# Optimization experiments

Measured on AMD Instinct MI355X. Metric: run time of the kernel, lower is better.

## Reference

```python
import jax, jax.numpy as jnp
import numpy as np

N_NODES = 100_000
N_EDGES = 1_200_000
C = 64            # channel_count
NF = 3            # node features
EF = 2            # edge features
ITERS = 5         # message passing iterations
VAR_EPS = 1e-5


def _mlp(x, W1, b1, W2, b2):
    # NeuralNetwork(in, out, hidden_count=1, hidden_size): in->hidden, relu, hidden->out
    return jax.nn.relu(x @ W1 + b1) @ W2 + b2


def setup_inputs() -> dict:
    key = jax.random.key(0)
    ks = jax.random.split(key, 20)

    def glorot(k, shape):
        fan_in = shape[0]
        return jax.random.normal(k, shape, dtype=jnp.float32) / jnp.sqrt(jnp.float32(fan_in))

    msg_in = EF + 2 * C           # 130
    upd_in = 4 * C + C            # 320 (4 aggregators + node embedding)
    ro_in = 2 * C + EF            # 130

    return {
        "node_features": jax.random.normal(ks[0], (N_NODES, NF), dtype=jnp.float32),
        "edge_features": jax.random.normal(ks[1], (N_EDGES, EF), dtype=jnp.float32),
        "init_W": glorot(ks[2], (NF, C)),
        "init_b": jnp.zeros((C,), jnp.float32),
        "msg_W1": glorot(ks[3], (msg_in, C)),
        "msg_b1": jnp.zeros((C,), jnp.float32),
        "msg_W2": glorot(ks[4], (C, C)),
        "msg_b2": jnp.zeros((C,), jnp.float32),
        "upd_W1": glorot(ks[5], (upd_in, C)),
        "upd_b1": jnp.zeros((C,), jnp.float32),
        "upd_W2": glorot(ks[6], (C, C)),
        "upd_b2": jnp.zeros((C,), jnp.float32),
        "ro_W1": glorot(ks[7], (ro_in, C)),
        "ro_b1": jnp.zeros((C,), jnp.float32),
        "ro_W2": glorot(ks[8], (C, 1)),
        "ro_b2": jnp.zeros((1,), jnp.float32),
        "edge_index": jax.random.randint(ks[9], (2, N_EDGES), 0, N_NODES, dtype=jnp.int32),
    }


def reference(node_features, edge_features, init_W, init_b,
              msg_W1, msg_b1, msg_W2, msg_b2,
              upd_W1, upd_b1, upd_W2, upd_b2,
              ro_W1, ro_b1, ro_W2, ro_b2, edge_index):
    src = edge_index[0]  # j: sender
    dst = edge_index[1]  # i: receiver (PyG source_to_target flow)

    ones = jnp.ones((src.shape[0], 1), jnp.float32)
    cnt = jax.ops.segment_sum(ones, dst, num_segments=N_NODES)      # [N,1]
    cnt_c = jnp.maximum(cnt, 1.0)
    has_edge = cnt > 0

    emb = node_features @ init_W + init_b  # [N,C]
    for _ in range(ITERS):
        h = jax.nn.relu(emb)
        # message: cat(x_i, x_j, edge_features) -> MLP
        m = _mlp(jnp.concatenate([h[dst], h[src], edge_features], axis=1),
                 msg_W1, msg_b1, msg_W2, msg_b2)                    # [E,C]
        s = jax.ops.segment_sum(m, dst, num_segments=N_NODES)
        mean = s / cnt_c
        mean2 = jax.ops.segment_sum(m * m, dst, num_segments=N_NODES) / cnt_c
        std = jnp.sqrt(jax.nn.relu(mean2 - mean * mean) + VAR_EPS)
        mn = jnp.where(has_edge, jax.ops.segment_min(m, dst, num_segments=N_NODES), 0.0)
        mx = jnp.where(has_edge, jax.ops.segment_max(m, dst, num_segments=N_NODES), 0.0)
        agg = jnp.concatenate([std, mn, mx, mean], axis=1)           # [N,4C]
        # update: cat(aggregated, node_embeddings) -> MLP
        emb = _mlp(jnp.concatenate([agg, h], axis=1),
                   upd_W1, upd_b1, upd_W2, upd_b2)

    # readout per edge: cat(emb[attacker], emb[attacked], edge_features)
    ro_in = jnp.concatenate([emb[src], emb[dst], edge_features], axis=1)
    return _mlp(ro_in, ro_W1, ro_b1, ro_W2, ro_b2)                   # [E,1]
```

## Files before the change

### kernel.cpp

```cpp
#include <hip/hip_runtime.h>

#define NN 100000
#define NE 1200000
#define ITERS 5
#define NTILES (NE/16)
#define TPW 16
#define NWAVES ((NTILES+TPW-1)/TPW)
#define NBLK_E ((NWAVES+3)/4)
#define NBLK_U ((NN+63)/64)

typedef __attribute__((ext_vector_type(8))) short short8;
typedef __attribute__((ext_vector_type(4))) short short4_t;
typedef __attribute__((ext_vector_type(4))) float floatx4;
typedef unsigned short ushort_t;

__device__ inline ushort_t f2bf(float f){
  unsigned u = __float_as_uint(f);
  unsigned r = (u + 0x7fffu + ((u>>16)&1u)) >> 16;
  return (ushort_t)r;
}
__device__ inline float bf2f(ushort_t u){ return __uint_as_float(((unsigned)u)<<16); }
__device__ inline float bf2f_lo(unsigned u){ return __uint_as_float(u<<16); }
__device__ inline float bf2f_hi(unsigned u){ return __uint_as_float(u & 0xffff0000u); }

__device__ inline int xcd_swz(int orig, int nwg){
  int q = nwg >> 3, r = nwg & 7;
  int x = orig & 7, i = orig >> 3;
  return (x < r ? x*(q+1) : r*(q+1) + (x-r)*q) + i;
}

__global__ void k_count(const int* __restrict__ dst, int* __restrict__ cnt){
  int base = (blockIdx.x*256 + threadIdx.x)*4;
  if (base >= NE) return;
  int4 d4 = *reinterpret_cast<const int4*>(dst + base);
  atomicAdd(&cnt[d4.x],1); atomicAdd(&cnt[d4.y],1);
  atomicAdd(&cnt[d4.z],1); atomicAdd(&cnt[d4.w],1);
}

__global__ void k_scan1(const int* __restrict__ cnt, int* __restrict__ bsum){
  __shared__ int s[256];
  int t = threadIdx.x; int i = blockIdx.x*256 + t;
  s[t] = (i < NN) ? cnt[i] : 0; __syncthreads();
  for (int off=128; off>0; off>>=1){ if (t<off) s[t]+=s[t+off]; __syncthreads(); }
  if (t==0) bsum[blockIdx.x] = s[0];
}

__global__ void k_scan2(int* bsum, int nb){
  __shared__ int s[512];
  int t = threadIdx.x;
  int v = (t<nb)? bsum[t] : 0;
  s[t]=v; __syncthreads();
  for (int off=1; off<512; off<<=1){
    int x = (t>=off)? s[t-off] : 0; __syncthreads();
    s[t]+=x; __syncthreads();
  }
  if (t<nb) bsum[t] = s[t]-v;
}

__global__ void k_scan3(const int* __restrict__ cnt, const int* __restrict__ bsum, int* __restrict__ rowptr){
  __shared__ int s[256];
  int t=threadIdx.x; int i = blockIdx.x*256+t;
  int v = (i<NN)? cnt[i]:0;
  s[t]=v; __syncthreads();
  for (int off=1; off<256; off<<=1){
    int x = (t>=off)? s[t-off] : 0; __syncthreads();
    s[t] += x; __syncthreads();
  }
  if (i<NN) rowptr[i] = bsum[blockIdx.x] + s[t] - v;
  if (i==0) rowptr[NN] = NE;
}

__global__ void k_filldst(const int* __restrict__ rowptr, int* __restrict__ dsts){
  int n = blockIdx.x*256 + threadIdx.x;
  if (n >= NN) return;
  int a = rowptr[n], b = rowptr[n+1];
  for (int p = a; p < b; ++p) dsts[p] = n;
}

__global__ void k_scatter(const int* __restrict__ src, const int* __restrict__ dst,
                          const float* __restrict__ ef,
                          int* __restrict__ fill,
                          int2* __restrict__ edges){
  int e = blockIdx.x*256+threadIdx.x;
  if (e>=NE) return;
  int d = dst[e];
  float2 f = reinterpret_cast<const float2*>(ef)[e];
  int sv = src[e];
  int pos = atomicAdd(&fill[d],1);
  edges[pos] = make_int2(sv, (int)((unsigned)f2bf(f.x)|((unsigned)f2bf(f.y)<<16)));
}

__global__ void k_wprep(const float* __restrict__ W, ushort_t* __restrict__ frag, int Ksrc, int total){
  int t = blockIdx.x*256+threadIdx.x;
  if (t>=total) return;
  int j = t&7, l=(t>>3)&63, ct=(t>>9)&3, ks=t>>11;
  int k = ks*32 + ((l>>4)<<3) + j;
  int col = ct*16 + (l&15);
  float v = (k<Ksrc)? W[k*64+col] : 0.f;
  frag[t] = f2bf(v);
}

__global__ void k_init(const float* __restrict__ nf, const float* __restrict__ W, const float* __restrict__ b,
                       ushort_t* __restrict__ hA, ushort_t* __restrict__ emb){
  int t = blockIdx.x*256+threadIdx.x;
  if (t >= NN*64) return;
  int n=t>>6, c=t&63;
  float a = b[c];
  a += nf[n*3+0]*W[0*64+c];
  a += nf[n*3+1]*W[1*64+c];
  a += nf[n*3+2]*W[2*64+c];
  emb[t] = f2bf(a);
  hA[t] = f2bf(fmaxf(a,0.f));
}

__launch_bounds__(256)
__global__ void k_edge(const ushort_t* __restrict__ h,
                       const int2* __restrict__ edges, const int* __restrict__ dsts,
                       const ushort_t* __restrict__ w1f, const ushort_t* __restrict__ w2f,
                       const float* __restrict__ b1, const float* __restrict__ b2,
                       ushort_t* __restrict__ m_s){
  int tid = threadIdx.x;
  int wv = tid>>6, lane = tid&63;
  int lo = lane&15, hi = lane>>4;
  int wave = xcd_swz(blockIdx.x, NBLK_E)*4 + wv;
  int t0 = wave*TPW;
  if (t0 >= NTILES) return;
  int t1 = t0 + TPW; if (t1 > NTILES) t1 = NTILES;

  const short8* w1 = reinterpret_cast<const short8*>(w1f) + lane;
  const short8* w2 = reinterpret_cast<const short8*>(w2f) + lane;

  float bb1[4][4], bb2s[4][4];
  #pragma unroll
  for (int ct=0;ct<4;ct++)
    #pragma unroll
    for (int jr=0;jr<4;jr++){
      bb1[ct][jr]  = b1[ct*16 + hi*4 + jr];
      bb2s[ct][jr] = b2[ct*16 + hi*4 + jr];
    }

  int2 recA = edges[t0*16 + lo];
  int  dvA  = dsts[t0*16 + lo];
  short8 cg0 = *reinterpret_cast<const short8*>(h + (size_t)dvA*64 + hi*8);
  short8 cg1 = *reinterpret_cast<const short8*>(h + (size_t)dvA*64 + (4+hi)*8);
  short8 cg2 = *reinterpret_cast<const short8*>(h + (size_t)recA.x*64 + hi*8);
  short8 cg3 = *reinterpret_cast<const short8*>(h + (size_t)recA.x*64 + (4+hi)*8);
  int tB = (t0+1 < t1)? t0+1 : t0;
  int2 recB = edges[tB*16 + lo];
  int  dvB  = dsts[tB*16 + lo];

  for (int t = t0; t < t1; ++t){
    short8 ng0 = *reinterpret_cast<const short8*>(h + (size_t)dvB*64 + hi*8);
    short8 ng1 = *reinterpret_cast<const short8*>(h + (size_t)dvB*64 + (4+hi)*8);
    short8 ng2 = *reinterpret_cast<const short8*>(h + (size_t)recB.x*64 + hi*8);
    short8 ng3 = *reinterpret_cast<const short8*>(h + (size_t)recB.x*64 + (4+hi)*8);
    int tC = (t+2 < t1)? t+2 : ((t+1 < t1)? t+1 : t);
    int2 recC = edges[tC*16 + lo];
    int  dvC  = dsts[tC*16 + lo];

    unsigned ev = (unsigned)recA.y;
    short8 b4v = {0,0,0,0,0,0,0,0};
    if (hi==0){ b4v[0] = (short)(ev & 0xffffu); b4v[1] = (short)(ev >> 16); }

    floatx4 a1[4];
    #pragma unroll
    for (int ct=0;ct<4;ct++) a1[ct]=(floatx4){bb1[ct][0],bb1[ct][1],bb1[ct][2],bb1[ct][3]};
    __builtin_amdgcn_s_setprio(1);
    #pragma unroll
    for (int ct=0;ct<4;ct++) a1[ct] = __builtin_amdgcn_mfma_f32_16x16x32_bf16(w1[(0*4+ct)*64], cg0, a1[ct],0,0,0);
    #pragma unroll
    for (int ct=0;ct<4;ct++) a1[ct] = __builtin_amdgcn_mfma_f32_16x16x32_bf16(w1[(1*4+ct)*64], cg1, a1[ct],0,0,0);
    #pragma unroll
    for (int ct=0;ct<4;ct++) a1[ct] = __builtin_amdgcn_mfma_f32_16x16x32_bf16(w1[(2*4+ct)*64], cg2, a1[ct],0,0,0);
    #pragma unroll
    for (int ct=0;ct<4;ct++) a1[ct] = __builtin_amdgcn_mfma_f32_16x16x32_bf16(w1[(3*4+ct)*64], cg3, a1[ct],0,0,0);
    #pragma unroll
    for (int ct=0;ct<4;ct++) a1[ct] = __builtin_amdgcn_mfma_f32_16x16x32_bf16(w1[(4*4+ct)*64], b4v, a1[ct],0,0,0);
    __builtin_amdgcn_s_setprio(0);

    short8 ha0, ha1;
    #pragma unroll
    for (int jj=0;jj<8;jj++){
      int Ls = ((lane&16)<<1) | ((jj>>2)<<4) | lo;
      float va = __shfl(a1[0][jj&3], Ls);
      float vb = __shfl(a1[1][jj&3], Ls);
      float v0 = (lane>=32)? vb : va;
      ha0[jj] = (short)f2bf(fmaxf(v0,0.f));
      float vc = __shfl(a1[2][jj&3], Ls);
      float vd = __shfl(a1[3][jj&3], Ls);
      float v1 = (lane>=32)? vd : vc;
      ha1[jj] = (short)f2bf(fmaxf(v1,0.f));
    }

    floatx4 mt[4];
    #pragma unroll
    for (int ct=0;ct<4;ct++) mt[ct]=(floatx4){bb2s[ct][0],bb2s[ct][1],bb2s[ct][2],bb2s[ct][3]};
    __builtin_amdgcn_s_setprio(1);
    #pragma unroll
    for (int ct=0;ct<4;ct++) mt[ct] = __builtin_amdgcn_mfma_f32_16x16x32_bf16(w2[(0*4+ct)*64], ha0, mt[ct],0,0,0);
    #pragma unroll
    for (int ct=0;ct<4;ct++) mt[ct] = __builtin_amdgcn_mfma_f32_16x16x32_bf16(w2[(1*4+ct)*64], ha1, mt[ct],0,0,0);
    __builtin_amdgcn_s_setprio(0);

    #pragma unroll
    for (int ct=0;ct<4;ct++){
      short4_t pk = {(short)f2bf(mt[ct][0]), (short)f2bf(mt[ct][1]),
                     (short)f2bf(mt[ct][2]), (short)f2bf(mt[ct][3])};
      *reinterpret_cast<short4_t*>(m_s + (size_t)(t*16+lo)*64 + ct*16 + hi*4) = pk;
    }

    recA = recB; dvA = dvB; recB = recC; dvB = dvC;
    cg0 = ng0; cg1 = ng1; cg2 = ng2; cg3 = ng3;
  }
}

__launch_bounds__(256)
__global__ void k_update(const ushort_t* __restrict__ m_s,
                         const int* __restrict__ rowptr,
                         const ushort_t* __restrict__ hin,
                         const ushort_t* __restrict__ w1f, const ushort_t* __restrict__ w2f,
                         const float* __restrict__ b1, const float* __restrict__ b2,
                         ushort_t* __restrict__ emb, ushort_t* __restrict__ hout){
  __shared__ short xl[4*10*64*8];
  int n0 = xcd_swz(blockIdx.x, NBLK_U)*64;
  int tid = threadIdx.x;
  int wv = tid>>6, lane = tid&63;
  int b = lane>>4;
  int c4 = (lane&15)*4;
  int n0w = n0 + wv*16;

  int rp_l;
  {
    int o = lane; if (o > 17) o = 17;
    int idx = n0w + o; if (idx > NN) idx = NN;
    rp_l = rowptr[idx];
  }

  for (int batch=0; batch<4; batch++){
    int q = batch*4 + b;
    int n = n0w + q;
    bool nv = n < NN;
    int rp0 = __shfl(rp_l, q);
    int rp1 = __shfl(rp_l, q+1);
    int deg = rp1 - rp0;

    float sm0=0.f,sm1=0.f,sm2=0.f,sm3=0.f;
    float sq0=0.f,sq1=0.f,sq2=0.f,sq3=0.f;
    float mn0=3.4e38f,mn1=3.4e38f,mn2=3.4e38f,mn3=3.4e38f;
    float mx0=-3.4e38f,mx1=-3.4e38f,mx2=-3.4e38f,mx3=-3.4e38f;

    const ushort_t* mp = m_s + (size_t)rp0*64 + c4;

#define ACC4(U) { \
      float v0=bf2f_lo((U).x), v1=bf2f_hi((U).x), v2=bf2f_lo((U).y), v3=bf2f_hi((U).y); \
      sm0+=v0; sq0+=v0*v0; mn0=fminf(mn0,v0); mx0=fmaxf(mx0,v0); \
      sm1+=v1; sq1+=v1*v1; mn1=fminf(mn1,v1); mx1=fmaxf(mx1,v1); \
      sm2+=v2; sq2+=v2*v2; mn2=fminf(mn2,v2); mx2=fmaxf(mx2,v2); \
      sm3+=v3; sq3+=v3*v3; mn3=fminf(mn3,v3); mx3=fmaxf(mx3,v3); }

    int i = 0;
    for (; i + 2 <= deg; i += 2){
      uint2 ua = *reinterpret_cast<const uint2*>(mp + (size_t)i*64);
      uint2 ub = *reinterpret_cast<const uint2*>(mp + (size_t)(i+1)*64);
      ACC4(ua); ACC4(ub);
    }
    if (i < deg){
      uint2 ua = *reinterpret_cast<const uint2*>(mp + (size_t)i*64);
      ACC4(ua);
    }
#undef ACC4

    float invc = 1.f / (float)(deg>0?deg:1);
    float me0=sm0*invc, me1=sm1*invc, me2=sm2*invc, me3=sm3*invc;
    float sd0=__fsqrt_rn(fmaxf(sq0*invc-me0*me0,0.f)+1e-5f);
    float sd1=__fsqrt_rn(fmaxf(sq1*invc-me1*me1,0.f)+1e-5f);
    float sd2=__fsqrt_rn(fmaxf(sq2*invc-me2*me2,0.f)+1e-5f);
    float sd3=__fsqrt_rn(fmaxf(sq3*invc-me3*me3,0.f)+1e-5f);
    if (deg<=0){ mn0=mn1=mn2=mn3=0.f; mx0=mx1=mx2=mx3=0.f; }

    auto stw = [&](int s, short4_t val){
      int k0 = s*64 + c4;
      int ks = k0>>5, g2=(k0>>3)&3, j0 = c4&7;
      *reinterpret_cast<short4_t*>(&xl[(((wv*10+ks)*64 + g2*16 + q)<<3) + j0]) = val;
    };
    stw(0, (short4_t){(short)f2bf(sd0),(short)f2bf(sd1),(short)f2bf(sd2),(short)f2bf(sd3)});
    stw(1, (short4_t){(short)f2bf(mn0),(short)f2bf(mn1),(short)f2bf(mn2),(short)f2bf(mn3)});
    stw(2, (short4_t){(short)f2bf(mx0),(short)f2bf(mx1),(short)f2bf(mx2),(short)f2bf(mx3)});
    stw(3, (short4_t){(short)f2bf(me0),(short)f2bf(me1),(short)f2bf(me2),(short)f2bf(me3)});
    uint2 hu = {0u,0u};
    if (nv) hu = *reinterpret_cast<const uint2*>(hin + (size_t)n*64 + c4);
    stw(4, (short4_t){(short)(hu.x&0xffffu),(short)(hu.x>>16),(short)(hu.y&0xffffu),(short)(hu.y>>16)});
  }
  __syncthreads();

  int r0 = (lane>>4)*4;
  const short8* xw = reinterpret_cast<const short8*>(xl) + wv*10*64 + lane;
  const short8* w1 = reinterpret_cast<const short8*>(w1f) + lane;
  floatx4 acc[4];
  #pragma unroll
  for (int ct=0;ct<4;ct++){ float bb=b1[ct*16+(lane&15)]; acc[ct]=(floatx4){bb,bb,bb,bb}; }
  #pragma unroll
  for (int ks=0; ks<10; ks++){
    short8 a = xw[ks*64];
    #pragma unroll
    for (int ct=0;ct<4;ct++)
      acc[ct] = __builtin_amdgcn_mfma_f32_16x16x32_bf16(a, w1[(ks*4+ct)*64], acc[ct], 0,0,0);
  }
  __syncthreads();
  #pragma unroll
  for (int ct=0; ct<4; ct++){
    int colk = ct*16 + (lane&15);
    int ks2 = colk>>5, g2=(colk>>3)&3, j2=colk&7;
    #pragma unroll
    for (int j=0;j<4;j++)
      xl[(((wv*10+ks2)*64 + g2*16 + (r0+j))<<3) + j2] = (short)f2bf(fmaxf(acc[ct][j],0.f));
  }
  __syncthreads();

  const short8* w2 = reinterpret_cast<const short8*>(w2f) + lane;
  floatx4 mac[4];
  #pragma unroll
  for (int ct=0;ct<4;ct++){ float bb=b2[ct*16+(lane&15)]; mac[ct]=(floatx4){bb,bb,bb,bb}; }
  #pragma unroll
  for (int ks=0; ks<2; ks++){
    short8 a = xw[ks*64];
    #pragma unroll
    for (int ct=0;ct<4;ct++)
      mac[ct] = __builtin_amdgcn_mfma_f32_16x16x32_bf16(a, w2[(ks*4+ct)*64], mac[ct], 0,0,0);
  }
  #pragma unroll
  for (int ct=0;ct<4;ct++){
    int col = ct*16+(lane&15);
    #pragma unroll
    for (int j=0;j<4;j++){
      int n = n0 + wv*16 + r0 + j;
      if (n < NN){
        float v = mac[ct][j];
        emb[(size_t)n*64+col] = f2bf(v);
        hout[(size_t)n*64+col] = f2bf(fmaxf(v,0.f));
      }
    }
  }
}

__launch_bounds__(256)
__global__ void k_readout(const ushort_t* __restrict__ emb,
                          const int* __restrict__ srcI, const int* __restrict__ dstI,
                          const float* __restrict__ ef,
                          const ushort_t* __restrict__ w1f,
                          const float* __restrict__ b1,
                          const float* __restrict__ w2, const float* __restrict__ b2,
                          float* __restrict__ out){
  int tid = threadIdx.x;
  int wv = tid>>6, lane = tid&63;
  int lo = lane&15, g = lane>>4;
  int wave = blockIdx.x*4 + wv;
  int t0 = wave*TPW;
  if (t0 >= NTILES) return;
  int t1 = t0 + TPW; if (t1 > NTILES) t1 = NTILES;

  const short8* w1 = reinterpret_cast<const short8*>(w1f) + lane;
  float bia[4];
  #pragma unroll
  for (int ct=0;ct<4;ct++) bia[ct] = b1[ct*16+lo];
  float w2v[4];
  #pragma unroll
  for (int ct=0;ct<4;ct++) w2v[ct] = w2[ct*16+lo];
  float bb2 = b2[0];
  int r0 = g*4;

  int pA = t0*16 + lo;
  int svA = srcI[pA], dvA = dstI[pA];
  float2 fA = reinterpret_cast<const float2*>(ef)[pA];
  short8 v0_ = *reinterpret_cast<const short8*>(emb + (size_t)svA*64 + g*8);
  short8 v1_ = *reinterpret_cast<const short8*>(emb + (size_t)svA*64 + (4+g)*8);
  short8 v2_ = *reinterpret_cast<const short8*>(emb + (size_t)dvA*64 + g*8);
  short8 v3_ = *reinterpret_cast<const short8*>(emb + (size_t)dvA*64 + (4+g)*8);
  int tB = (t0+1 < t1)? t0+1 : t0;
  int pB = tB*16 + lo;
  int svB = srcI[pB], dvB = dstI[pB];
  float2 fB = reinterpret_cast<const float2*>(ef)[pB];

  for (int t = t0; t < t1; ++t){
    short8 n0 = *reinterpret_cast<const short8*>(emb + (size_t)svB*64 + g*8);
    short8 n1 = *reinterpret_cast<const short8*>(emb + (size_t)svB*64 + (4+g)*8);
    short8 n2 = *reinterpret_cast<const short8*>(emb + (size_t)dvB*64 + g*8);
    short8 n3 = *reinterpret_cast<const short8*>(emb + (size_t)dvB*64 + (4+g)*8);
    int tC = (t+2 < t1)? t+2 : ((t+1 < t1)? t+1 : t);
    int pC = tC*16 + lo;
    int svC = srcI[pC], dvC = dstI[pC];
    float2 fC = reinterpret_cast<const float2*>(ef)[pC];

    unsigned evc = (unsigned)f2bf(fA.x) | ((unsigned)f2bf(fA.y)<<16);
    short8 b4v = {0,0,0,0,0,0,0,0};
    if (g==0){ b4v[0] = (short)(evc & 0xffffu); b4v[1] = (short)(evc >> 16); }

    floatx4 acc[4];
    #pragma unroll
    for (int ct=0;ct<4;ct++) acc[ct]=(floatx4){bia[ct],bia[ct],bia[ct],bia[ct]};
    __builtin_amdgcn_s_setprio(1);
    #pragma unroll
    for (int ct=0;ct<4;ct++) acc[ct] = __builtin_amdgcn_mfma_f32_16x16x32_bf16(v0_, w1[(0*4+ct)*64], acc[ct],0,0,0);
    #pragma unroll
    for (int ct=0;ct<4;ct++) acc[ct] = __builtin_amdgcn_mfma_f32_16x16x32_bf16(v1_, w1[(1*4+ct)*64], acc[ct],0,0,0);
    #pragma unroll
    for (int ct=0;ct<4;ct++) acc[ct] = __builtin_amdgcn_mfma_f32_16x16x32_bf16(v2_, w1[(2*4+ct)*64], acc[ct],0,0,0);
    #pragma unroll
    for (int ct=0;ct<4;ct++) acc[ct] = __builtin_amdgcn_mfma_f32_16x16x32_bf16(v3_, w1[(3*4+ct)*64], acc[ct],0,0,0);
    #pragma unroll
    for (int ct=0;ct<4;ct++) acc[ct] = __builtin_amdgcn_mfma_f32_16x16x32_bf16(b4v, w1[(4*4+ct)*64], acc[ct],0,0,0);
    __builtin_amdgcn_s_setprio(0);

    float part[4];
    #pragma unroll
    for (int j=0;j<4;j++){
      float pj = 0.f;
      #pragma unroll
      for (int ct=0;ct<4;ct++) pj += fmaxf(acc[ct][j],0.f)*w2v[ct];
      part[j] = pj;
    }
    #pragma unroll
    for (int m=1;m<16;m<<=1){
      #pragma unroll
      for (int j=0;j<4;j++) part[j] += __shfl_xor(part[j], m, 64);
    }
    if (lo==0){
      float4 o = make_float4(part[0]+bb2, part[1]+bb2, part[2]+bb2, part[3]+bb2);
      *reinterpret_cast<float4*>(out + t*16 + r0) = o;
    }

    v0_=n0; v1_=n1; v2_=n2; v3_=n3;
    fA = fB; fB = fC;
    svB = svC; dvB = dvC;
  }
}

extern "C" void kernel_launch(void* const* d_in, const int* in_sizes, int n_in,
                              void* d_out, int out_size, void* d_ws, size_t ws_size,
                              hipStream_t stream){
  const float* nf    = (const float*)d_in[0];
  const float* ef    = (const float*)d_in[1];
  const float* initW = (const float*)d_in[2];
  const float* initb = (const float*)d_in[3];
  const float* msgW1 = (const float*)d_in[4];
  const float* msgb1 = (const float*)d_in[5];
  const float* msgW2 = (const float*)d_in[6];
  const float* msgb2 = (const float*)d_in[7];
  const float* updW1 = (const float*)d_in[8];
  const float* updb1 = (const float*)d_in[9];
  const float* updW2 = (const float*)d_in[10];
  const float* updb2 = (const float*)d_in[11];
  const float* roW1  = (const float*)d_in[12];
  const float* rob1  = (const float*)d_in[13];
  const float* roW2  = (const float*)d_in[14];
  const float* rob2  = (const float*)d_in[15];
  const int*   eidx  = (const int*)d_in[16];
  const int* srcI = eidx;
  const int* dstI = eidx + NE;
  float* out = (float*)d_out;

  char* base = (char*)d_ws; size_t off = 0;
  auto alloc = [&](size_t b)->char*{ char* p = base + off; off = (off + b + 255) & ~(size_t)255; return p; };
  int* cnt    = (int*)alloc((size_t)NN*4);
  int* fill   = (int*)alloc((size_t)NN*4);
  int* rowptr = (int*)alloc((size_t)(NN+1)*4);
  int* bsum   = (int*)alloc(512*4);
  int2* edges = (int2*)alloc((size_t)NE*8);
  int* dsts   = (int*)alloc((size_t)NE*4);
  ushort_t* hA  = (ushort_t*)alloc((size_t)NN*64*2);
  ushort_t* hB  = (ushort_t*)alloc((size_t)NN*64*2);
  ushort_t* emb = (ushort_t*)alloc((size_t)NN*64*2);
  ushort_t* m_s = (ushort_t*)alloc((size_t)NE*64*2);
  ushort_t* msgW1f = (ushort_t*)alloc(5*2048*2);
  ushort_t* msgW2f = (ushort_t*)alloc(2*2048*2);
  ushort_t* updW1f = (ushort_t*)alloc(10*2048*2);
  ushort_t* updW2f = (ushort_t*)alloc(2*2048*2);
  ushort_t* roW1f  = (ushort_t*)alloc(5*2048*2);
  (void)ws_size; (void)in_sizes; (void)n_in; (void)out_size;

  hipMemsetAsync(cnt, 0, (size_t)NN*4, stream);
  int nb = (NN+255)/256;
  k_count<<<(NE/4+255)/256,256,0,stream>>>(dstI,cnt);
  k_scan1<<<nb,256,0,stream>>>(cnt,bsum);
  k_scan2<<<1,512,0,stream>>>(bsum,nb);
  k_scan3<<<nb,256,0,stream>>>(cnt,bsum,rowptr);
  hipMemcpyAsync(fill, rowptr, (size_t)NN*4, hipMemcpyDeviceToDevice, stream);
  k_filldst<<<nb,256,0,stream>>>(rowptr,dsts);
  k_scatter<<<(NE+255)/256,256,0,stream>>>(srcI,dstI,ef,fill,edges);
  k_wprep<<<(5*2048+255)/256,256,0,stream>>>(msgW1,msgW1f,130,5*2048);
  k_wprep<<<(2*2048+255)/256,256,0,stream>>>(msgW2,msgW2f,64,2*2048);
  k_wprep<<<(10*2048+255)/256,256,0,stream>>>(updW1,updW1f,320,10*2048);
  k_wprep<<<(2*2048+255)/256,256,0,stream>>>(updW2,updW2f,64,2*2048);
  k_wprep<<<(5*2048+255)/256,256,0,stream>>>(roW1,roW1f,130,5*2048);
  k_init<<<(NN*64+255)/256,256,0,stream>>>(nf,initW,initb,hA,emb);

  for (int it=0; it<ITERS; it++){
    const ushort_t* hin = (it&1)? hB : hA;
    ushort_t* hout      = (it&1)? hA : hB;
    k_edge<<<NBLK_E,256,0,stream>>>(hin,edges,dsts,msgW1f,msgW2f,msgb1,msgb2,m_s);
    k_update<<<NBLK_U,256,0,stream>>>(m_s,rowptr,hin,updW1f,updW2f,updb1,updb2,emb,hout);
  }
  k_readout<<<NBLK_E,256,0,stream>>>(emb,srcI,dstI,ef,roW1f,rob1,roW2,rob2,out);
}
```

Before: 847.6 us.

## Replace global-atomic edge scatter with two-pass bucketed binning; tune edge kernel occupancy

The single-pass CSR scatter, which did one global atomic per edge into random node slots, is replaced by two passes. First, edges are binned into 512-node buckets through a shared-memory histogram with one global atomic per bucket per block. A second kernel then scatters each bucket's edges into final positions, where atomics and writes stay localized. The edge kernel also gains a waves-per-EU launch bound and loads biases as vector reads per tile instead of holding them in registers, trading a 16-byte temp buffer and an extra pass for better locality.

```diff
diff --git a/kernel.cpp b/kernel.cpp
--- a/kernel.cpp
+++ b/kernel.cpp
@@ -8,6 +8,9 @@
 #define NWAVES ((NTILES+TPW-1)/TPW)
 #define NBLK_E ((NWAVES+3)/4)
 #define NBLK_U ((NN+63)/64)
+#define NBUK ((NN+511)/512)
+#define BINSZ 4096
+#define NBLK_BIN ((NE+BINSZ-1)/BINSZ)
 
 typedef __attribute__((ext_vector_type(8))) short short8;
 typedef __attribute__((ext_vector_type(4))) short short4_t;
@@ -77,17 +80,59 @@
   for (int p = a; p < b; ++p) dsts[p] = n;
 }
 
-__global__ void k_scatter(const int* __restrict__ src, const int* __restrict__ dst,
-                          const float* __restrict__ ef,
-                          int* __restrict__ fill,
-                          int2* __restrict__ edges){
-  int e = blockIdx.x*256+threadIdx.x;
-  if (e>=NE) return;
-  int d = dst[e];
-  float2 f = reinterpret_cast<const float2*>(ef)[e];
-  int sv = src[e];
-  int pos = atomicAdd(&fill[d],1);
-  edges[pos] = make_int2(sv, (int)((unsigned)f2bf(f.x)|((unsigned)f2bf(f.y)<<16)));
+__global__ void k_binit(const int* __restrict__ rowptr, int* __restrict__ bfill){
+  int b = blockIdx.x*256 + threadIdx.x;
+  if (b >= NBUK) return;
+  int n = b*512; if (n > NN) n = NN;
+  bfill[b] = rowptr[n];
+}
+
+__global__ void k_bin(const int* __restrict__ src, const int* __restrict__ dst,
+                      const float* __restrict__ ef,
+                      int* __restrict__ bfill, int4* __restrict__ btmp){
+  __shared__ int hist[NBUK];
+  __shared__ int base[NBUK];
+  int t = threadIdx.x;
+  for (int i=t; i<NBUK; i+=256) hist[i]=0;
+  __syncthreads();
+  int e0 = blockIdx.x*BINSZ + t;
+  #pragma unroll
+  for (int k=0;k<BINSZ/256;k++){
+    int e = e0 + k*256;
+    if (e < NE) atomicAdd(&hist[dst[e]>>9], 1);
+  }
+  __syncthreads();
+  for (int i=t; i<NBUK; i+=256){
+    int c = hist[i];
+    base[i] = (c>0)? atomicAdd(&bfill[i], c) : 0;
+    hist[i] = 0;
+  }
+  __syncthreads();
+  #pragma unroll
+  for (int k=0;k<BINSZ/256;k++){
+    int e = e0 + k*256;
+    if (e < NE){
+      int d = dst[e];
+      int b = d>>9;
+      int off = atomicAdd(&hist[b],1);
+      float2 f = reinterpret_cast<const float2*>(ef)[e];
+      int efp = (int)((unsigned)f2bf(f.x)|((unsigned)f2bf(f.y)<<16));
+      btmp[base[b]+off] = make_int4(src[e], d, efp, 0);
+    }
+  }
+}
+
+__global__ void k_sort2(const int4* __restrict__ btmp, const int* __restrict__ rowptr,
+                        int* __restrict__ fill, int2* __restrict__ edges){
+  int b = blockIdx.x;
+  int nlo = b*512; if (nlo > NN) nlo = NN;
+  int nhi = (b+1)*512; if (nhi > NN) nhi = NN;
+  int plo = rowptr[nlo], phi = rowptr[nhi];
+  for (int p = plo + threadIdx.x; p < phi; p += 256){
+    int4 r = btmp[p];
+    int pos = atomicAdd(&fill[r.y],1);
+    edges[pos] = make_int2(r.x, r.z);
+  }
 }
 
 __global__ void k_wprep(const float* __restrict__ W, ushort_t* __restrict__ frag, int Ksrc, int total){
@@ -113,7 +158,7 @@
   hA[t] = f2bf(fmaxf(a,0.f));
 }
 
-__launch_bounds__(256)
+__launch_bounds__(256, 6)
 __global__ void k_edge(const ushort_t* __restrict__ h,
                        const int2* __restrict__ edges, const int* __restrict__ dsts,
                        const ushort_t* __restrict__ w1f, const ushort_t* __restrict__ w2f,
@@ -129,15 +174,8 @@
 
   const short8* w1 = reinterpret_cast<const short8*>(w1f) + lane;
   const short8* w2 = reinterpret_cast<const short8*>(w2f) + lane;
-
-  float bb1[4][4], bb2s[4][4];
-  #pragma unroll
-  for (int ct=0;ct<4;ct++)
-    #pragma unroll
-    for (int jr=0;jr<4;jr++){
-      bb1[ct][jr]  = b1[ct*16 + hi*4 + jr];
-      bb2s[ct][jr] = b2[ct*16 + hi*4 + jr];
-    }
+  const floatx4* b1v = reinterpret_cast<const floatx4*>(b1);
+  const floatx4* b2v = reinterpret_cast<const floatx4*>(b2);
 
   int2 recA = edges[t0*16 + lo];
   int  dvA  = dsts[t0*16 + lo];
@@ -164,7 +202,7 @@
 
     floatx4 a1[4];
     #pragma unroll
-    for (int ct=0;ct<4;ct++) a1[ct]=(floatx4){bb1[ct][0],bb1[ct][1],bb1[ct][2],bb1[ct][3]};
+    for (int ct=0;ct<4;ct++) a1[ct] = b1v[ct*4 + hi];
     __builtin_amdgcn_s_setprio(1);
     #pragma unroll
     for (int ct=0;ct<4;ct++) a1[ct] = __builtin_amdgcn_mfma_f32_16x16x32_bf16(w1[(0*4+ct)*64], cg0, a1[ct],0,0,0);
@@ -194,7 +232,7 @@
 
     floatx4 mt[4];
     #pragma unroll
-    for (int ct=0;ct<4;ct++) mt[ct]=(floatx4){bb2s[ct][0],bb2s[ct][1],bb2s[ct][2],bb2s[ct][3]};
+    for (int ct=0;ct<4;ct++) mt[ct] = b2v[ct*4 + hi];
     __builtin_amdgcn_s_setprio(1);
     #pragma unroll
     for (int ct=0;ct<4;ct++) mt[ct] = __builtin_amdgcn_mfma_f32_16x16x32_bf16(w2[(0*4+ct)*64], ha0, mt[ct],0,0,0);
@@ -465,6 +503,8 @@
   int* fill   = (int*)alloc((size_t)NN*4);
   int* rowptr = (int*)alloc((size_t)(NN+1)*4);
   int* bsum   = (int*)alloc(512*4);
+  int* bfill  = (int*)alloc((size_t)NBUK*4);
+  int4* btmp  = (int4*)alloc((size_t)NE*16);
   int2* edges = (int2*)alloc((size_t)NE*8);
   int* dsts   = (int*)alloc((size_t)NE*4);
   ushort_t* hA  = (ushort_t*)alloc((size_t)NN*64*2);
@@ -486,7 +526,9 @@
   k_scan3<<<nb,256,0,stream>>>(cnt,bsum,rowptr);
   hipMemcpyAsync(fill, rowptr, (size_t)NN*4, hipMemcpyDeviceToDevice, stream);
   k_filldst<<<nb,256,0,stream>>>(rowptr,dsts);
-  k_scatter<<<(NE+255)/256,256,0,stream>>>(srcI,dstI,ef,fill,edges);
+  k_binit<<<(NBUK+255)/256,256,0,stream>>>(rowptr,bfill);
+  k_bin<<<NBLK_BIN,256,0,stream>>>(srcI,dstI,ef,bfill,btmp);
+  k_sort2<<<NBUK,256,0,stream>>>(btmp,rowptr,fill,edges);
   k_wprep<<<(5*2048+255)/256,256,0,stream>>>(msgW1,msgW1f,130,5*2048);
   k_wprep<<<(2*2048+255)/256,256,0,stream>>>(msgW2,msgW2f,64,2*2048);
   k_wprep<<<(10*2048+255)/256,256,0,stream>>>(updW1,updW1f,320,10*2048);
```

Result: slower. 2.950 ms (+248.1%).
